# Kernel optimization log

Hardware: AMD Instinct MI355X
Metric: run time of the kernel (lower is better)

The kernel has to match this reference:

```python
import jax, jax.numpy as jnp
import numpy as np

ALPHA = 0.9
EPS = 1e-12
INIT_VALS = (0.001, 0.0001)


def setup_inputs() -> dict:
    key = jax.random.key(0)
    x = jax.random.normal(key, (16, 2000, 481, 2), dtype=jnp.float32)
    return {"x": x}


def reference(x):
    # x: [B, T, F, 2] (real/imag)
    B, T, F, _ = x.shape
    step = (INIT_VALS[1] - INIT_VALS[0]) / (F - 1)
    s0 = INIT_VALS[0] + jnp.arange(F, dtype=x.dtype) * step  # [F]
    s0 = jnp.broadcast_to(s0[None, :], (B, F))               # [B, F]

    x_abs = jnp.sqrt(x[..., 0] ** 2 + x[..., 1] ** 2)        # [B, T, F]

    def ema_step(s, xa_t):
        # s, xa_t: [B, F]
        s = ALPHA * s + (1.0 - ALPHA) * xa_t
        inv = 1.0 / jnp.sqrt(s + EPS)
        return s, inv

    # scan over time axis: move T to front
    _, inv = jax.lax.scan(ema_step, s0, jnp.moveaxis(x_abs, 1, 0))  # inv: [T, B, F]
    inv = jnp.moveaxis(inv, 0, 1)                                   # [B, T, F]

    # normalize both real and imag parts by the same rsqrt(s + eps)
    return x * inv[..., None]  # [B, T, F, 2]
```

## Files before the change

### kernel.cpp

```cpp
#include <hip/hip_runtime.h>
#include <math.h>


#define ALPHA 0.9f
#define OMA   0.1f
#define EPS_  1e-12f

typedef float vf4 __attribute__((ext_vector_type(4), aligned(8)));
typedef float vf2 __attribute__((ext_vector_type(2), aligned(8)));

constexpr int B_ = 16, T_ = 2000, F_ = 481;
constexpr int NCH = 16, LOOKBACK = 128;
constexpr int OUT0 = 245, OUTN = 117;
constexpr int ROWF = 2 * F_;

__global__ __launch_bounds__(256)
void specnorm_kernel(const float* __restrict__ x, float* __restrict__ out,
                     float* __restrict__ ws) {
    const int tid = threadIdx.x;
    if (tid > 240) return;
    const int chunk = blockIdx.x;
    const int b = blockIdx.y;
    const bool hasB = (tid < 240);

    const float step = (float)((0.0001 - 0.001) / (double)(F_ - 1));
    float sA = 0.001f + (float)(2 * tid) * step;
    float sB = 0.001f + (float)(2 * tid + 1) * step;

    const int tout0 = (chunk == 0) ? 0 : OUT0 + (chunk - 1) * OUTN;
    const int nout  = (chunk == 0) ? OUT0 : OUTN;
    const int nwarm = (chunk == 0) ? 0 : LOOKBACK;
    const int tstart = tout0 - nwarm;

    const float* xp = x + (size_t)(b * T_ + tstart) * ROWF + 4 * tid;
    float* opA = out + (size_t)(b * T_ + tout0) * ROWF + 4 * tid;
    float* opB = hasB ? (opA + 2) : (ws + 2 * (size_t)tid);
    const ptrdiff_t strideB = hasB ? ROWF : 0;

    #pragma unroll 8
    for (int t = 0; t < nwarm; ++t) {
        vf4 v = *(const vf4*)xp;
        float aA = __builtin_amdgcn_sqrtf(v.x * v.x + v.y * v.y);
        float aB = __builtin_amdgcn_sqrtf(v.z * v.z + v.w * v.w);
        sA = ALPHA * sA + OMA * aA;
        sB = ALPHA * sB + OMA * aB;
        xp += ROWF;
    }

    #pragma unroll 8
    for (int t = 0; t < nout; ++t) {
        vf4 v = *(const vf4*)xp;
        float aA = __builtin_amdgcn_sqrtf(v.x * v.x + v.y * v.y);
        float aB = __builtin_amdgcn_sqrtf(v.z * v.z + v.w * v.w);
        sA = ALPHA * sA + OMA * aA;
        sB = ALPHA * sB + OMA * aB;
        float iA = __builtin_amdgcn_rsqf(sA + EPS_);
        float iB = __builtin_amdgcn_rsqf(sB + EPS_);
        vf2 oA = { v.x * iA, v.y * iA };
        vf2 oB = { v.z * iB, v.w * iB };
        __builtin_nontemporal_store(oA, (vf2*)opA);
        __builtin_nontemporal_store(oB, (vf2*)opB);
        xp += ROWF;
        opA += ROWF;
        opB += strideB;
    }
}

extern "C" void kernel_launch(void* const* d_in, const int* in_sizes, int n_in,
                              void* d_out, int out_size, void* d_ws, size_t ws_size,
                              hipStream_t stream) {
    const float* x = (const float*)d_in[0];
    float* out = (float*)d_out;
    float* ws = (float*)d_ws;

    dim3 grid(NCH, B_);
    dim3 block(256);
    specnorm_kernel<<<grid, block, 0, stream>>>(x, out, ws);
}
```

Baseline: 246.7 us.

## Software-pipeline row loads with 8-deep register double buffering in EMA scan

Both the warmup and output loops now prefetch the next 8 time rows into a second set of registers while the current 8 are processed, so more loads are in flight per thread in this latency-bound sequential scan. Chunk sizes are changed to 200 and 120 so the step counts are multiples of 8. The two vf2 stores are merged into one vf4 store for full threads, and the dummy workspace store path for the last lane is removed. The cost is higher register use, which the launch bounds hint of one block per SM accepts.

```diff
diff --git a/kernel.cpp b/kernel.cpp
--- a/kernel.cpp
+++ b/kernel.cpp
@@ -11,10 +11,52 @@
 
 constexpr int B_ = 16, T_ = 2000, F_ = 481;
 constexpr int NCH = 16, LOOKBACK = 128;
-constexpr int OUT0 = 245, OUTN = 117;
+constexpr int OUT0 = 200, OUTN = 120;
 constexpr int ROWF = 2 * F_;
 
-__global__ __launch_bounds__(256)
+#define LD8(V) do { \
+  V##0 = *(const vf4*)(xp + 0 * ROWF); \
+  V##1 = *(const vf4*)(xp + 1 * ROWF); \
+  V##2 = *(const vf4*)(xp + 2 * ROWF); \
+  V##3 = *(const vf4*)(xp + 3 * ROWF); \
+  V##4 = *(const vf4*)(xp + 4 * ROWF); \
+  V##5 = *(const vf4*)(xp + 5 * ROWF); \
+  V##6 = *(const vf4*)(xp + 6 * ROWF); \
+  V##7 = *(const vf4*)(xp + 7 * ROWF); \
+  xp += 8 * ROWF; \
+} while (0)
+
+#define EMA1(v) do { \
+  float aA = __builtin_amdgcn_sqrtf((v).x * (v).x + (v).y * (v).y); \
+  float aB = __builtin_amdgcn_sqrtf((v).z * (v).z + (v).w * (v).w); \
+  sA = ALPHA * sA + OMA * aA; \
+  sB = ALPHA * sB + OMA * aB; \
+} while (0)
+
+#define EMA8(V) do { EMA1(V##0); EMA1(V##1); EMA1(V##2); EMA1(V##3); \
+                     EMA1(V##4); EMA1(V##5); EMA1(V##6); EMA1(V##7); } while (0)
+
+#define OUT1(v) do { \
+  EMA1(v); \
+  float iA = __builtin_amdgcn_rsqf(sA + EPS_); \
+  float iB = __builtin_amdgcn_rsqf(sB + EPS_); \
+  if (hasB) { \
+    vf4 o = { (v).x * iA, (v).y * iA, (v).z * iB, (v).w * iB }; \
+    __builtin_nontemporal_store(o, (vf4*)op); \
+  } else { \
+    vf2 o = { (v).x * iA, (v).y * iA }; \
+    __builtin_nontemporal_store(o, (vf2*)op); \
+  } \
+  op += ROWF; \
+} while (0)
+
+#define OUT8(V) do { OUT1(V##0); OUT1(V##1); OUT1(V##2); OUT1(V##3); \
+                     OUT1(V##4); OUT1(V##5); OUT1(V##6); OUT1(V##7); } while (0)
+
+#define CP8() do { a0 = b0; a1 = b1; a2 = b2; a3 = b3; \
+                   a4 = b4; a5 = b5; a6 = b6; a7 = b7; } while (0)
+
+__global__ __launch_bounds__(256, 1)
 void specnorm_kernel(const float* __restrict__ x, float* __restrict__ out,
                      float* __restrict__ ws) {
     const int tid = threadIdx.x;
@@ -33,37 +75,29 @@
     const int tstart = tout0 - nwarm;
 
     const float* xp = x + (size_t)(b * T_ + tstart) * ROWF + 4 * tid;
-    float* opA = out + (size_t)(b * T_ + tout0) * ROWF + 4 * tid;
-    float* opB = hasB ? (opA + 2) : (ws + 2 * (size_t)tid);
-    const ptrdiff_t strideB = hasB ? ROWF : 0;
+    float* op = out + (size_t)(b * T_ + tout0) * ROWF + 4 * tid;
+    (void)ws;
 
-    #pragma unroll 8
-    for (int t = 0; t < nwarm; ++t) {
-        vf4 v = *(const vf4*)xp;
-        float aA = __builtin_amdgcn_sqrtf(v.x * v.x + v.y * v.y);
-        float aB = __builtin_amdgcn_sqrtf(v.z * v.z + v.w * v.w);
-        sA = ALPHA * sA + OMA * aA;
-        sB = ALPHA * sB + OMA * aB;
-        xp += ROWF;
+    vf4 a0, a1, a2, a3, a4, a5, a6, a7;
+    vf4 b0, b1, b2, b3, b4, b5, b6, b7;
+
+    if (nwarm > 0) {
+        LD8(a);
+        for (int t = 8; t < LOOKBACK; t += 8) {
+            LD8(b);
+            EMA8(a);
+            CP8();
+        }
+        EMA8(a);
     }
 
-    #pragma unroll 8
-    for (int t = 0; t < nout; ++t) {
-        vf4 v = *(const vf4*)xp;
-        float aA = __builtin_amdgcn_sqrtf(v.x * v.x + v.y * v.y);
-        float aB = __builtin_amdgcn_sqrtf(v.z * v.z + v.w * v.w);
-        sA = ALPHA * sA + OMA * aA;
-        sB = ALPHA * sB + OMA * aB;
-        float iA = __builtin_amdgcn_rsqf(sA + EPS_);
-        float iB = __builtin_amdgcn_rsqf(sB + EPS_);
-        vf2 oA = { v.x * iA, v.y * iA };
-        vf2 oB = { v.z * iB, v.w * iB };
-        __builtin_nontemporal_store(oA, (vf2*)opA);
-        __builtin_nontemporal_store(oB, (vf2*)opB);
-        xp += ROWF;
-        opA += ROWF;
-        opB += strideB;
+    LD8(a);
+    for (int t = 8; t < nout; t += 8) {
+        LD8(b);
+        OUT8(a);
+        CP8();
     }
+    OUT8(a);
 }
 
 extern "C" void kernel_launch(void* const* d_in, const int* in_sizes, int n_in,
```

Result: faster. 236.8 us (-4.0%).
